# Performance work log

Hardware: AMD Instinct MI355X
Metric: run time of the kernel (lower is better)

## Reference

```python
import jax, jax.numpy as jnp
import numpy as np

EMBED_DIM = 1024
NUM_HEADS = 16
HEAD_DIM = EMBED_DIM // NUM_HEADS
SCALING_FACTOR = 0.1
SCALING = (HEAD_DIM * SCALING_FACTOR) ** (-0.5)
B, L = 4, 1024


def setup_inputs() -> dict:
    key = jax.random.key(0)
    ks = jax.random.split(key, 8)
    query = jax.random.normal(ks[0], (B, L, EMBED_DIM), dtype=jnp.float32)
    key_padding_mask = jnp.zeros((B, L), dtype=bool)
    attn_bias = jax.random.normal(ks[1], (B * NUM_HEADS, L, L), dtype=jnp.float32)
    s_in = 1.0 / np.sqrt(EMBED_DIM)
    Wqkv = jax.random.normal(ks[2], (3 * EMBED_DIM, EMBED_DIM), dtype=jnp.float32) * s_in
    bqkv = jnp.zeros((3 * EMBED_DIM,), dtype=jnp.float32)
    Wo = jax.random.normal(ks[3], (EMBED_DIM, EMBED_DIM), dtype=jnp.float32) * s_in
    bo = jnp.zeros((EMBED_DIM,), dtype=jnp.float32)
    return {"query": query, "key_padding_mask": key_padding_mask, "attn_bias": attn_bias,
            "Wqkv": Wqkv, "bqkv": bqkv, "Wo": Wo, "bo": bo}


def reference(query, key_padding_mask, attn_bias, Wqkv, bqkv, Wo, bo):
    b, l, e = query.shape
    # fused in-projection: (B, L, 3E)
    qkv = jnp.einsum("ble,fe->blf", query, Wqkv) + bqkv
    q, k, v = jnp.split(qkv, 3, axis=-1)
    q = q * SCALING
    # (B, L, H, D)
    q = q.reshape(b, l, NUM_HEADS, HEAD_DIM)
    k = k.reshape(b, l, NUM_HEADS, HEAD_DIM)
    v = v.reshape(b, l, NUM_HEADS, HEAD_DIM)
    # scores: (B, H, L, L)
    scores = jnp.einsum("blhd,bmhd->bhlm", q, k)
    scores = scores + attn_bias.reshape(b, NUM_HEADS, l, l)
    neg_inf = jnp.asarray(-jnp.inf, scores.dtype)
    scores = jnp.where(key_padding_mask[:, None, None, :], neg_inf, scores)
    probs = jax.nn.softmax(scores, axis=-1)  # dropout: eval mode (identity)
    out = jnp.einsum("bhlm,bmhd->blhd", probs, v).reshape(b, l, e)
    return jnp.einsum("ble,fe->blf", out, Wo) + bo
```

## Files before the change

### kernel.cpp

```cpp
#include <hip/hip_runtime.h>
#include <math.h>

#define EMB   1024
#define NH    16
#define HD    64
#define BATCH 4
#define LSEQ  1024
#define NTOK  (BATCH*LSEQ)
#define SCALING 0.39528470752104744f

typedef __attribute__((ext_vector_type(8))) short short8;
typedef __attribute__((ext_vector_type(4))) float f32x4;

__device__ __forceinline__ float bf2f(short s) {
    union { float f; unsigned u; } x; x.u = ((unsigned)(unsigned short)s) << 16; return x.f;
}
__device__ __forceinline__ short f2bf(float f) {
    union { float f; unsigned u; } x; x.f = f;
    unsigned r = x.u + 0x7fff + ((x.u >> 16) & 1);
    return (short)(r >> 16);
}

__device__ __forceinline__ void glds16(const void* g, void* l) {
    __builtin_amdgcn_global_load_lds(
        (const __attribute__((address_space(1))) void*)g,
        (__attribute__((address_space(3))) void*)l, 16, 0, 0);
}

__global__ __launch_bounds__(256) void cvt_bf16(
    const float* __restrict__ in, short* __restrict__ out, int n)
{
    int i = (blockIdx.x * 256 + threadIdx.x) * 8;
    if (i >= n) return;
    float4 a = *(const float4*)(in + i);
    float4 b = *(const float4*)(in + i + 4);
    short8 o;
    o[0] = f2bf(a.x); o[1] = f2bf(a.y); o[2] = f2bf(a.z); o[3] = f2bf(a.w);
    o[4] = f2bf(b.x); o[5] = f2bf(b.y); o[6] = f2bf(b.z); o[7] = f2bf(b.w);
    *(short8*)(out + i) = o;
}

__global__ __launch_bounds__(256) void qkv_gemm(
    const short* __restrict__ X, const short* __restrict__ W,
    const float* __restrict__ bqkv,
    short* __restrict__ qws, short* __restrict__ kws, short* __restrict__ vws)
{
    __shared__ short As[128 * 32];
    __shared__ short Bs[128 * 32];
    const int tid = threadIdx.x;
    const int wave = tid >> 6, lane = tid & 63;
    const int quad = lane >> 4, l16 = lane & 15;
    const int m0 = blockIdx.y * 128, n0 = blockIdx.x * 128;
    const int wm = (wave >> 1) * 64, wn = (wave & 1) * 64;

    f32x4 acc[4][4] = {};

    const int srow = wave * 16 + (lane >> 2);
    const int scol = (lane & 3) * 16;

    const char* gA = (const char*)X + (size_t)(m0 + srow) * 2048 + scol;
    const char* gB = (const char*)W + (size_t)(n0 + srow) * 2048 + scol;
    char* lA = (char*)As + wave * 1024 + lane * 16;
    char* lB = (char*)Bs + wave * 1024 + lane * 16;

    for (int kt = 0; kt < 1024; kt += 32) {
        __syncthreads();
        const char* ga = gA + kt * 2;
        const char* gb = gB + kt * 2;
        glds16(ga, lA);
        glds16(ga + (size_t)64 * 2048, lA + 4096);
        glds16(gb, lB);
        glds16(gb + (size_t)64 * 2048, lB + 4096);
        __syncthreads();

        short8 af[4], bf[4];
        #pragma unroll
        for (int i = 0; i < 4; i++)
            af[i] = *(const short8*)((const char*)As + (wm + i * 16 + l16) * 64 + quad * 16);
        #pragma unroll
        for (int j = 0; j < 4; j++)
            bf[j] = *(const short8*)((const char*)Bs + (wn + j * 16 + l16) * 64 + quad * 16);
        #pragma unroll
        for (int i = 0; i < 4; i++)
            #pragma unroll
            for (int j = 0; j < 4; j++)
                acc[i][j] = __builtin_amdgcn_mfma_f32_16x16x32_bf16(af[i], bf[j], acc[i][j], 0, 0, 0);
    }

    #pragma unroll
    for (int i = 0; i < 4; i++) {
        #pragma unroll
        for (int j = 0; j < 4; j++) {
            #pragma unroll
            for (int r = 0; r < 4; r++) {
                int gm = m0 + wm + i * 16 + quad * 4 + r;
                int gn = n0 + wn + j * 16 + l16;
                float v = acc[i][j][r] + bqkv[gn];
                int part = gn >> 10;
                int cc = gn & 1023;
                int h = cc >> 6, d = cc & 63;
                int b = gm >> 10, l = gm & 1023;
                size_t dst = (((size_t)(b * NH + h)) * LSEQ + l) * HD + d;
                if (part == 0)      qws[dst] = f2bf(v * SCALING);
                else if (part == 1) kws[dst] = f2bf(v);
                else                vws[dst] = f2bf(v);
            }
        }
    }
}

__global__ __launch_bounds__(256) void attn_kernel(
    const short* __restrict__ qws, const short* __restrict__ kws,
    const short* __restrict__ vws, const float* __restrict__ bias,
    const unsigned char* __restrict__ mask, short* __restrict__ att)
{
    __shared__ short Qs[64 * 72];
    __shared__ short Ks[128 * 72];
    __shared__ short Vt[64 * 136];
    __shared__ short Ps[4 * 16 * 136];

    const int qt = blockIdx.x;
    const int bh = blockIdx.y;
    const int b = bh >> 4;
    const int tid = threadIdx.x, wave = tid >> 6, lane = tid & 63;
    const int quad = lane >> 4, l16 = lane & 15;
    const int h = bh & 15;

    const short* Qg = qws + (size_t)bh * LSEQ * HD + (size_t)qt * 64 * HD;
    const short* Kg = kws + (size_t)bh * LSEQ * HD;
    const short* Vg = vws + (size_t)bh * LSEQ * HD;
    const float* Bg = bias + (size_t)bh * LSEQ * LSEQ;

    #pragma unroll
    for (int i = 0; i < 2; i++) {
        int c = i * 256 + tid;
        int row = c >> 3, col8 = c & 7;
        *(int4*)((char*)Qs + row * 144 + col8 * 16) =
            *(const int4*)((const char*)Qg + row * 128 + col8 * 16);
    }

    float m_r[4], l_r[4];
    f32x4 o[4] = {};
    #pragma unroll
    for (int r = 0; r < 4; r++) { m_r[r] = -INFINITY; l_r[r] = 0.0f; }

    const int qrow_g = qt * 64 + wave * 16 + quad * 4;

    for (int kt0 = 0; kt0 < LSEQ; kt0 += 128) {
        __syncthreads();
        #pragma unroll
        for (int i = 0; i < 4; i++) {
            int c = i * 256 + tid;
            int row = c >> 3, col8 = c & 7;
            *(int4*)((char*)Ks + row * 144 + col8 * 16) =
                *(const int4*)((const char*)Kg + (size_t)(kt0 + row) * 128 + col8 * 16);
        }
        #pragma unroll
        for (int i = 0; i < 4; i++) {
            int c = i * 256 + tid;
            int row = c >> 3, col8 = c & 7;
            short8 v = *(const short8*)(Vg + (size_t)(kt0 + row) * HD + col8 * 8);
            #pragma unroll
            for (int j = 0; j < 8; j++)
                Vt[(col8 * 8 + j) * 136 + row] = v[j];
        }
        __syncthreads();

        short8 qf[2];
        #pragma unroll
        for (int ks = 0; ks < 2; ks++)
            qf[ks] = *(const short8*)((const char*)Qs + (wave * 16 + l16) * 144 + ks * 64 + quad * 16);
        f32x4 s[8] = {};
        #pragma unroll
        for (int ni = 0; ni < 8; ni++) {
            #pragma unroll
            for (int ks = 0; ks < 2; ks++) {
                short8 kf = *(const short8*)((const char*)Ks + (ni * 16 + l16) * 144 + ks * 64 + quad * 16);
                s[ni] = __builtin_amdgcn_mfma_f32_16x16x32_bf16(qf[ks], kf, s[ni], 0, 0, 0);
            }
        }

        #pragma unroll
        for (int ni = 0; ni < 8; ni++) {
            int col = kt0 + ni * 16 + l16;
            bool mk = mask[(size_t)b * LSEQ + col] != 0;
            #pragma unroll
            for (int r = 0; r < 4; r++) {
                float bv = Bg[(size_t)(qrow_g + r) * LSEQ + col];
                float val = s[ni][r] + bv;
                s[ni][r] = mk ? -INFINITY : val;
            }
        }

        #pragma unroll
        for (int r = 0; r < 4; r++) {
            float mx = s[0][r];
            #pragma unroll
            for (int ni = 1; ni < 8; ni++) mx = fmaxf(mx, s[ni][r]);
            #pragma unroll
            for (int off = 1; off < 16; off <<= 1)
                mx = fmaxf(mx, __shfl_xor(mx, off, 64));
            float mnew = fmaxf(m_r[r], mx);
            float alpha = (m_r[r] == -INFINITY) ? 0.0f : __expf(m_r[r] - mnew);
            m_r[r] = mnew;
            float sum = 0.0f;
            #pragma unroll
            for (int ni = 0; ni < 8; ni++) {
                float p = __expf(s[ni][r] - mnew);
                s[ni][r] = p;
                sum += p;
            }
            #pragma unroll
            for (int off = 1; off < 16; off <<= 1)
                sum += __shfl_xor(sum, off, 64);
            l_r[r] = l_r[r] * alpha + sum;
            #pragma unroll
            for (int ni2 = 0; ni2 < 4; ni2++) o[ni2][r] *= alpha;
            #pragma unroll
            for (int ni = 0; ni < 8; ni++)
                Ps[wave * 2176 + (quad * 4 + r) * 136 + ni * 16 + l16] = f2bf(s[ni][r]);
        }

        #pragma unroll
        for (int ks = 0; ks < 4; ks++) {
            short8 pf = *(const short8*)((const char*)Ps + wave * 4352 + l16 * 272 + ks * 64 + quad * 16);
            #pragma unroll
            for (int ni2 = 0; ni2 < 4; ni2++) {
                short8 vf = *(const short8*)((const char*)Vt + (ni2 * 16 + l16) * 272 + ks * 64 + quad * 16);
                o[ni2] = __builtin_amdgcn_mfma_f32_16x16x32_bf16(pf, vf, o[ni2], 0, 0, 0);
            }
        }
    }

    #pragma unroll
    for (int r = 0; r < 4; r++) {
        float inv = 1.0f / l_r[r];
        int lq = qt * 64 + wave * 16 + quad * 4 + r;
        #pragma unroll
        for (int ni2 = 0; ni2 < 4; ni2++) {
            int d = ni2 * 16 + l16;
            att[((size_t)(b * LSEQ + lq)) * EMB + h * HD + d] = f2bf(o[ni2][r] * inv);
        }
    }
}

__global__ __launch_bounds__(256) void out_gemm(
    const short* __restrict__ Xa, const short* __restrict__ Wo,
    const float* __restrict__ bo, float* __restrict__ out)
{
    __shared__ short As[128 * 32];
    __shared__ short Bs[128 * 32];
    const int tid = threadIdx.x;
    const int wave = tid >> 6, lane = tid & 63;
    const int quad = lane >> 4, l16 = lane & 15;
    const int m0 = blockIdx.y * 128, n0 = blockIdx.x * 128;
    const int wm = (wave >> 1) * 64, wn = (wave & 1) * 64;

    f32x4 acc[4][4] = {};

    const int srow = wave * 16 + (lane >> 2);
    const int scol = (lane & 3) * 16;
    const char* gA = (const char*)Xa + (size_t)(m0 + srow) * 2048 + scol;
    const char* gB = (const char*)Wo + (size_t)(n0 + srow) * 2048 + scol;
    char* lA = (char*)As + wave * 1024 + lane * 16;
    char* lB = (char*)Bs + wave * 1024 + lane * 16;

    for (int kt = 0; kt < 1024; kt += 32) {
        __syncthreads();
        const char* ga = gA + kt * 2;
        const char* gb = gB + kt * 2;
        glds16(ga, lA);
        glds16(ga + (size_t)64 * 2048, lA + 4096);
        glds16(gb, lB);
        glds16(gb + (size_t)64 * 2048, lB + 4096);
        __syncthreads();

        short8 af[4], bf[4];
        #pragma unroll
        for (int i = 0; i < 4; i++)
            af[i] = *(const short8*)((const char*)As + (wm + i * 16 + l16) * 64 + quad * 16);
        #pragma unroll
        for (int j = 0; j < 4; j++)
            bf[j] = *(const short8*)((const char*)Bs + (wn + j * 16 + l16) * 64 + quad * 16);
        #pragma unroll
        for (int i = 0; i < 4; i++)
            #pragma unroll
            for (int j = 0; j < 4; j++)
                acc[i][j] = __builtin_amdgcn_mfma_f32_16x16x32_bf16(af[i], bf[j], acc[i][j], 0, 0, 0);
    }

    #pragma unroll
    for (int i = 0; i < 4; i++) {
        #pragma unroll
        for (int j = 0; j < 4; j++) {
            #pragma unroll
            for (int r = 0; r < 4; r++) {
                int gm = m0 + wm + i * 16 + quad * 4 + r;
                int gn = n0 + wn + j * 16 + l16;
                out[(size_t)gm * EMB + gn] = acc[i][j][r] + bo[gn];
            }
        }
    }
}

extern "C" void kernel_launch(void* const* d_in, const int* in_sizes, int n_in,
                              void* d_out, int out_size, void* d_ws, size_t ws_size,
                              hipStream_t stream) {
    const float* query = (const float*)d_in[0];
    const unsigned char* mask = (const unsigned char*)d_in[1];
    const float* bias = (const float*)d_in[2];
    const float* Wqkv = (const float*)d_in[3];
    const float* bqkv = (const float*)d_in[4];
    const float* Wo   = (const float*)d_in[5];
    const float* bo   = (const float*)d_in[6];
    float* out = (float*)d_out;

    short* Xb  = (short*)d_ws;
    short* Wb  = Xb  + (size_t)4096 * 1024;
    short* Wob = Wb  + (size_t)3072 * 1024;
    short* qws = Wob + (size_t)1024 * 1024;
    short* kws = qws + (size_t)64 * 1024 * 64;
    short* vws = kws + (size_t)64 * 1024 * 64;
    short* att = vws + (size_t)64 * 1024 * 64;

    cvt_bf16<<<dim3(4096 * 1024 / 8 / 256), 256, 0, stream>>>(query, Xb, 4096 * 1024);
    cvt_bf16<<<dim3(3072 * 1024 / 8 / 256), 256, 0, stream>>>(Wqkv, Wb, 3072 * 1024);
    cvt_bf16<<<dim3(1024 * 1024 / 8 / 256), 256, 0, stream>>>(Wo, Wob, 1024 * 1024);

    qkv_gemm<<<dim3(24, 32), 256, 0, stream>>>(Xb, Wb, bqkv, qws, kws, vws);
    attn_kernel<<<dim3(16, 64), 256, 0, stream>>>(qws, kws, vws, bias, mask, att);
    out_gemm<<<dim3(8, 32), 256, 0, stream>>>(att, Wob, bo, out);
}
```

Before: 484.2 us.

## Store V transposed in QKV GEMM, prefetch bias into registers, remap attention blocks

The QKV GEMM epilogue now writes V transposed (head-dim major), so the attention kernel loads V tiles with vector copies instead of scalar LDS scatter-transposes. The attention bias and mask for the next key tile are loaded into registers during the current tile's softmax, overlapping the dominant fp32 bias stream with compute. Q fragments are loaded once and their LDS is shared with the P buffer. A flat grid remaps blocks so all query tiles of a head land on the same XCD for K/V cache reuse, and launch bounds request 3 blocks per CU. The costs are higher register pressure from the 32 prefetched bias values and strided scalar V stores in the GEMM epilogue.

```diff
diff --git a/kernel.cpp b/kernel.cpp
--- a/kernel.cpp
+++ b/kernel.cpp
@@ -57,7 +57,6 @@
 
     const int srow = wave * 16 + (lane >> 2);
     const int scol = (lane & 3) * 16;
-
     const char* gA = (const char*)X + (size_t)(m0 + srow) * 2048 + scol;
     const char* gB = (const char*)W + (size_t)(n0 + srow) * 2048 + scol;
     char* lA = (char*)As + wave * 1024 + lane * 16;
@@ -100,44 +99,50 @@
                 int cc = gn & 1023;
                 int h = cc >> 6, d = cc & 63;
                 int b = gm >> 10, l = gm & 1023;
-                size_t dst = (((size_t)(b * NH + h)) * LSEQ + l) * HD + d;
-                if (part == 0)      qws[dst] = f2bf(v * SCALING);
-                else if (part == 1) kws[dst] = f2bf(v);
-                else                vws[dst] = f2bf(v);
-            }
-        }
-    }
-}
-
-__global__ __launch_bounds__(256) void attn_kernel(
+                size_t bh = (size_t)(b * NH + h);
+                if (part == 0)      qws[(bh * LSEQ + l) * HD + d] = f2bf(v * SCALING);
+                else if (part == 1) kws[(bh * LSEQ + l) * HD + d] = f2bf(v);
+                else                vws[(bh * HD + d) * LSEQ + l] = f2bf(v);
+            }
+        }
+    }
+}
+
+__global__ __launch_bounds__(256, 3) void attn_kernel(
     const short* __restrict__ qws, const short* __restrict__ kws,
     const short* __restrict__ vws, const float* __restrict__ bias,
     const unsigned char* __restrict__ mask, short* __restrict__ att)
 {
-    __shared__ short Qs[64 * 72];
     __shared__ short Ks[128 * 72];
-    __shared__ short Vt[64 * 136];
-    __shared__ short Ps[4 * 16 * 136];
-
-    const int qt = blockIdx.x;
-    const int bh = blockIdx.y;
-    const int b = bh >> 4;
+    __shared__ short Vs[64 * 136];
+    __shared__ short PQ[4 * 2176];
+
+    const int flat = blockIdx.x;
+    const int xcd = flat & 7, ii = flat >> 3;
+    const int bh = xcd * 8 + (ii >> 4);
+    const int qt = ii & 15;
+    const int b = bh >> 4, h = bh & 15;
     const int tid = threadIdx.x, wave = tid >> 6, lane = tid & 63;
     const int quad = lane >> 4, l16 = lane & 15;
-    const int h = bh & 15;
 
     const short* Qg = qws + (size_t)bh * LSEQ * HD + (size_t)qt * 64 * HD;
     const short* Kg = kws + (size_t)bh * LSEQ * HD;
-    const short* Vg = vws + (size_t)bh * LSEQ * HD;
+    const short* Vg = vws + (size_t)bh * HD * LSEQ;
     const float* Bg = bias + (size_t)bh * LSEQ * LSEQ;
+    const unsigned char* Mg = mask + (size_t)b * LSEQ;
 
     #pragma unroll
     for (int i = 0; i < 2; i++) {
         int c = i * 256 + tid;
         int row = c >> 3, col8 = c & 7;
-        *(int4*)((char*)Qs + row * 144 + col8 * 16) =
+        *(int4*)((char*)PQ + row * 144 + col8 * 16) =
             *(const int4*)((const char*)Qg + row * 128 + col8 * 16);
     }
+    __syncthreads();
+    short8 qf[2];
+    #pragma unroll
+    for (int ks = 0; ks < 2; ks++)
+        qf[ks] = *(const short8*)((const char*)PQ + (wave * 16 + l16) * 144 + ks * 64 + quad * 16);
 
     float m_r[4], l_r[4];
     f32x4 o[4] = {};
@@ -145,6 +150,19 @@
     for (int r = 0; r < 4; r++) { m_r[r] = -INFINITY; l_r[r] = 0.0f; }
 
     const int qrow_g = qt * 64 + wave * 16 + quad * 4;
+
+    float bv[8][4];
+    float mkf[8];
+    #pragma unroll
+    for (int ni = 0; ni < 8; ni++) {
+        int col = ni * 16 + l16;
+        mkf[ni] = Mg[col] ? -INFINITY : 0.0f;
+        #pragma unroll
+        for (int r = 0; r < 4; r++)
+            bv[ni][r] = Bg[(size_t)(qrow_g + r) * LSEQ + col];
+    }
+
+    short* Pw = PQ + wave * 2176;
 
     for (int kt0 = 0; kt0 < LSEQ; kt0 += 128) {
         __syncthreads();
@@ -158,18 +176,12 @@
         #pragma unroll
         for (int i = 0; i < 4; i++) {
             int c = i * 256 + tid;
-            int row = c >> 3, col8 = c & 7;
-            short8 v = *(const short8*)(Vg + (size_t)(kt0 + row) * HD + col8 * 8);
-            #pragma unroll
-            for (int j = 0; j < 8; j++)
-                Vt[(col8 * 8 + j) * 136 + row] = v[j];
-        }
-        __syncthreads();
-
-        short8 qf[2];
-        #pragma unroll
-        for (int ks = 0; ks < 2; ks++)
-            qf[ks] = *(const short8*)((const char*)Qs + (wave * 16 + l16) * 144 + ks * 64 + quad * 16);
+            int row = c >> 4, col16 = c & 15;
+            *(int4*)((char*)Vs + row * 272 + col16 * 16) =
+                *(const int4*)((const char*)Vg + (size_t)row * 2048 + kt0 * 2 + col16 * 16);
+        }
+        __syncthreads();
+
         f32x4 s[8] = {};
         #pragma unroll
         for (int ni = 0; ni < 8; ni++) {
@@ -182,13 +194,19 @@
 
         #pragma unroll
         for (int ni = 0; ni < 8; ni++) {
-            int col = kt0 + ni * 16 + l16;
-            bool mk = mask[(size_t)b * LSEQ + col] != 0;
-            #pragma unroll
-            for (int r = 0; r < 4; r++) {
-                float bv = Bg[(size_t)(qrow_g + r) * LSEQ + col];
-                float val = s[ni][r] + bv;
-                s[ni][r] = mk ? -INFINITY : val;
+            #pragma unroll
+            for (int r = 0; r < 4; r++)
+                s[ni][r] = s[ni][r] + bv[ni][r] + mkf[ni];
+        }
+        if (kt0 + 128 < LSEQ) {
+            int nk = kt0 + 128;
+            #pragma unroll
+            for (int ni = 0; ni < 8; ni++) {
+                int col = nk + ni * 16 + l16;
+                mkf[ni] = Mg[col] ? -INFINITY : 0.0f;
+                #pragma unroll
+                for (int r = 0; r < 4; r++)
+                    bv[ni][r] = Bg[(size_t)(qrow_g + r) * LSEQ + col];
             }
         }
 
@@ -218,15 +236,15 @@
             for (int ni2 = 0; ni2 < 4; ni2++) o[ni2][r] *= alpha;
             #pragma unroll
             for (int ni = 0; ni < 8; ni++)
-                Ps[wave * 2176 + (quad * 4 + r) * 136 + ni * 16 + l16] = f2bf(s[ni][r]);
+                Pw[(quad * 4 + r) * 136 + ni * 16 + l16] = f2bf(s[ni][r]);
         }
 
         #pragma unroll
         for (int ks = 0; ks < 4; ks++) {
-            short8 pf = *(const short8*)((const char*)Ps + wave * 4352 + l16 * 272 + ks * 64 + quad * 16);
+            short8 pf = *(const short8*)((const char*)Pw + l16 * 272 + ks * 64 + quad * 16);
             #pragma unroll
             for (int ni2 = 0; ni2 < 4; ni2++) {
-                short8 vf = *(const short8*)((const char*)Vt + (ni2 * 16 + l16) * 272 + ks * 64 + quad * 16);
+                short8 vf = *(const short8*)((const char*)Vs + (ni2 * 16 + l16) * 272 + ks * 64 + quad * 16);
                 o[ni2] = __builtin_amdgcn_mfma_f32_16x16x32_bf16(pf, vf, o[ni2], 0, 0, 0);
             }
         }
@@ -328,6 +346,6 @@
     cvt_bf16<<<dim3(1024 * 1024 / 8 / 256), 256, 0, stream>>>(Wo, Wob, 1024 * 1024);
 
     qkv_gemm<<<dim3(24, 32), 256, 0, stream>>>(Xb, Wb, bqkv, qws, kws, vws);
-    attn_kernel<<<dim3(16, 64), 256, 0, stream>>>(qws, kws, vws, bias, mask, att);
+    attn_kernel<<<dim3(1024), 256, 0, stream>>>(qws, kws, vws, bias, mask, att);
     out_gemm<<<dim3(8, 32), 256, 0, stream>>>(att, Wob, bo, out);
 }
```

Measured after the change: 740.1 us. +52.9%, slower.
